# Kernel tuning notes

Hardware: AMD Instinct MI355X
Metric: run time of the kernel (lower is better)

## Reference

```python
import jax, jax.numpy as jnp
import numpy as np

BATCH = 4096
IN_DIM = 512
OUT_DIM = 512
GRID_SIZE = 5
K = 3


def _extended_grid():
    # Original: grid = linspace(-1, 1, grid_size+1), spacing h = 2/grid_size.
    # The de Boor-Cox recursion in the source indexes up to grid[grid_size+2k],
    # so we extend the uniform grid to the right with the same spacing.
    h = 2.0 / GRID_SIZE
    return (-1.0 + h * jnp.arange(GRID_SIZE + 2 * K + 1)).astype(jnp.float32)


def bspline_basis(x, grid, k):
    """Vectorized de Boor-Cox recursion.
    x: [..., ] floats; returns basis [..., grid_size + k].
    Identical math to the recursive b_spline_basis in the source, but computed
    bottom-up over all knot intervals at once (no redundant recomputation).
    """
    xe = x[..., None]  # [..., 1]
    # degree-0: indicator of half-open knot intervals, [..., n_knots-1]
    B = ((grid[:-1] <= xe) & (xe < grid[1:])).astype(x.dtype)
    for d in range(1, k + 1):
        n = grid.shape[0] - d - 1
        gi, gid = grid[:n], grid[d:d + n]          # grid[i], grid[i+d]
        gi1, gid1 = grid[1:n + 1], grid[d + 1:d + n + 1]  # grid[i+1], grid[i+d+1]
        # uniform grid -> denominators are d*h, never zero
        B = (xe - gi) / (gid - gi) * B[..., :n] + (gid1 - xe) / (gid1 - gi1) * B[..., 1:n + 1]
    return B  # [..., grid_size + k]


def setup_inputs() -> dict:
    key = jax.random.key(0)
    k1, k2 = jax.random.split(key)
    x = jax.random.uniform(k1, (BATCH, IN_DIM), jnp.float32) * 2.0 - 1.0  # in [-1, 1)
    spline_coeff = jax.random.normal(k2, (IN_DIM, OUT_DIM, GRID_SIZE + K), jnp.float32)
    spline_scaling = jnp.ones((IN_DIM, OUT_DIM), jnp.float32)
    return {"x": x, "spline_coeff": spline_coeff, "spline_scaling": spline_scaling}


def reference(x, spline_coeff, spline_scaling):
    grid = _extended_grid()
    basis = bspline_basis(x, grid, K)  # [B, in_dim, grid_size+k]
    # out[b, j] = sum_i scaling[i,j] * sum_g basis[b,i,g] * coeff[i,j,g]
    return jnp.einsum('big,ijg,ij->bj', basis, spline_coeff, spline_scaling)
```

## Files before the change

### kernel.cpp

```cpp
#include <hip/hip_runtime.h>
#include <hip/hip_bf16.h>
#include <stdint.h>


#define BATCH   4096
#define IN_DIM  512
#define OUT_DIM 512
#define KDIM    (IN_DIM * 8)
#define SPLITK  4
#define KSPAN   (KDIM / SPLITK)
#define NKS     (KSPAN / 64)

typedef short short8 __attribute__((ext_vector_type(8)));
typedef float f32x4  __attribute__((ext_vector_type(4)));

#define WAIT_VM8   0xF78
#define WAIT_VM0   0xF70
#define WAIT_LGKM0 0xC07F

__device__ __forceinline__ unsigned short f2bf(float f) {
  union { float f; unsigned int u; } v; v.f = f;
  unsigned int r = v.u + 0x7FFFu + ((v.u >> 16) & 1u);
  return (unsigned short)(r >> 16);
}

__device__ __forceinline__ void bspline_win(float xv, float* w, int* mm) {
  float t = (xv + 1.0f) * 2.5f;
  int m = (int)t;
  m = m < 0 ? 0 : (m > 4 ? 4 : m);
  float u  = t - (float)m;
  float u2 = u * u, u3 = u2 * u, om = 1.0f - u;
  w[0] = om * om * om * (1.0f / 6.0f);
  w[1] = (3.0f * u3 - 6.0f * u2 + 4.0f) * (1.0f / 6.0f);
  w[2] = (-3.0f * u3 + 3.0f * u2 + 3.0f * u + 1.0f) * (1.0f / 6.0f);
  w[3] = u3 * (1.0f / 6.0f);
  *mm = m;
}

__device__ __forceinline__ short8 basis_pack8(float xv) {
  float w[4]; int m;
  bspline_win(xv, w, &m);
  short8 h = {};
#pragma unroll
  for (int g = 0; g < 8; ++g) {
    int d = g - m + 3;
    float v = (d == 0) ? w[0] : (d == 1) ? w[1] : (d == 2) ? w[2] : (d == 3) ? w[3] : 0.0f;
    h[g] = (short)f2bf(v);
  }
  return h;
}

__device__ __forceinline__ void async_load16(const void* g, void* l) {
  __builtin_amdgcn_global_load_lds(
      (__attribute__((address_space(1))) void*)(uintptr_t)g,
      (__attribute__((address_space(3))) void*)(unsigned int)(uintptr_t)l,
      16, 0, 0);
}

__global__ void kan_prep(const float* __restrict__ x,
                         const float* __restrict__ coeff,
                         const float* __restrict__ scaling,
                         unsigned short* __restrict__ Ag,
                         unsigned short* __restrict__ Wt,
                         float* __restrict__ out) {
  const int b = blockIdx.x;
  const int NB_A = (BATCH * IN_DIM) / 256;
  const int NB_W = (IN_DIM * OUT_DIM) / 256;
  if (b < NB_A) {
    int idx = b * 256 + threadIdx.x;
    short8 h = basis_pack8(x[idx]);
    *reinterpret_cast<short8*>(Ag + (size_t)idx * 8) = h;
  } else if (b < NB_A + NB_W) {
    int idx = (b - NB_A) * 256 + threadIdx.x;
    int i = idx >> 9, j = idx & 511;
    float s = scaling[idx];
    const float4* cp = reinterpret_cast<const float4*>(coeff) + (size_t)idx * 2;
    float4 c0 = cp[0], c1 = cp[1];
    short8 h;
    h[0] = (short)f2bf(c0.x * s); h[1] = (short)f2bf(c0.y * s);
    h[2] = (short)f2bf(c0.z * s); h[3] = (short)f2bf(c0.w * s);
    h[4] = (short)f2bf(c1.x * s); h[5] = (short)f2bf(c1.y * s);
    h[6] = (short)f2bf(c1.z * s); h[7] = (short)f2bf(c1.w * s);
    *reinterpret_cast<short8*>(Wt + (size_t)j * KDIM + i * 8) = h;
  } else {
    size_t t = (size_t)(b - NB_A - NB_W) * 256 + threadIdx.x;
    reinterpret_cast<float4*>(out)[t] = make_float4(0.f, 0.f, 0.f, 0.f);
  }
}

__global__ __launch_bounds__(256, 2)
void kan_gemm_s(const unsigned short* __restrict__ Ag,
                const unsigned short* __restrict__ Wt,
                float* __restrict__ out) {
  __shared__ unsigned short As[2][128 * 64];
  __shared__ unsigned short Bs[2][128 * 64];

  const int tid  = threadIdx.x;
  const int lane = tid & 63;
  const int wid  = tid >> 6;
  const int wm = wid >> 1, wn = wid & 1;
  const int ln = lane & 15, quad = lane >> 4;

  const int b    = blockIdx.x;
  const int ks   = b & 3;
  const int mt   = (b >> 2) & 31;
  const int nt   = b >> 7;
  const int row0 = mt * 128;
  const int col0 = nt * 128;
  const int k0   = ks * KSPAN;

  f32x4 acc[4][4] = {};
  short8 af[2][4], bfr[2][4];

  const int lr = lane >> 3;
  const int cg = (lane & 7) ^ lr;

  const unsigned short* aRow = Ag + (size_t)(row0 + wid * 32 + lr) * KDIM + k0 + cg * 8;
  const unsigned short* bRow = Wt + (size_t)(col0 + wid * 32 + lr) * KDIM + k0 + cg * 8;

  auto issue = [&](int kt, int st) {
    const int kk0 = kt * 64;
#pragma unroll
    for (int t = 0; t < 4; ++t) {
      const int rbase = wid * 32 + t * 8;
      async_load16(aRow + (size_t)t * 8 * KDIM + kk0, &As[st][rbase * 64]);
      async_load16(bRow + (size_t)t * 8 * KDIM + kk0, &Bs[st][rbase * 64]);
    }
  };

  auto loadFrags = [&](int st) {
#pragma unroll
    for (int kk = 0; kk < 2; ++kk) {
#pragma unroll
      for (int m = 0; m < 4; ++m) {
        const int r    = wm * 64 + m * 16 + ln;
        const int slot = (kk * 4 + quad) ^ (r & 7);
        af[kk][m] = *reinterpret_cast<const short8*>(&As[st][r * 64 + slot * 8]);
      }
#pragma unroll
      for (int n = 0; n < 4; ++n) {
        const int c    = wn * 64 + n * 16 + ln;
        const int slot = (kk * 4 + quad) ^ (c & 7);
        bfr[kk][n] = *reinterpret_cast<const short8*>(&Bs[st][c * 64 + slot * 8]);
      }
    }
  };

  auto mfmaAll = [&]() {
#pragma unroll
    for (int kk = 0; kk < 2; ++kk)
#pragma unroll
      for (int m = 0; m < 4; ++m)
#pragma unroll
        for (int n = 0; n < 4; ++n)
          acc[m][n] = __builtin_amdgcn_mfma_f32_16x16x32_bf16(af[kk][m], bfr[kk][n], acc[m][n], 0, 0, 0);
  };

  issue(0, 0); issue(1, 1);

  for (int kt = 0; kt < NKS - 1; ++kt) {
    __builtin_amdgcn_s_waitcnt(WAIT_VM8);
    __builtin_amdgcn_s_barrier();
    loadFrags(kt & 1);
    __builtin_amdgcn_s_waitcnt(WAIT_LGKM0);
    __builtin_amdgcn_sched_barrier(0);
    __builtin_amdgcn_s_barrier();
    if (kt + 2 < NKS) issue(kt + 2, kt & 1);
    mfmaAll();
  }
  __builtin_amdgcn_s_waitcnt(WAIT_VM0);
  __builtin_amdgcn_s_barrier();
  loadFrags((NKS - 1) & 1);
  mfmaAll();

#pragma unroll
  for (int m = 0; m < 4; ++m)
#pragma unroll
    for (int n = 0; n < 4; ++n) {
      const int col = col0 + wn * 64 + n * 16 + ln;
#pragma unroll
      for (int r = 0; r < 4; ++r) {
        const int row = row0 + wm * 64 + m * 16 + quad * 4 + r;
        atomicAdd(&out[(size_t)row * OUT_DIM + col], acc[m][n][r]);
      }
    }
}

__global__ __launch_bounds__(256, 2)
void kan_gemm_fb(const float* __restrict__ x, const float* __restrict__ coeff,
                 const float* __restrict__ scaling, float* __restrict__ out) {
  __shared__ unsigned short As[64 * 64];
  __shared__ unsigned short Bs[64 * 64];

  const int tid  = threadIdx.x;
  const int lane = tid & 63;
  const int wid  = tid >> 6;
  const int wm = wid >> 1, wn = wid & 1;
  const int ln = lane & 15, quad = lane >> 4;
  const int row0 = blockIdx.y * 64;
  const int col0 = blockIdx.x * 64;

  f32x4 acc[2][2] = {};

  for (int kt = 0; kt < KDIM / 64; ++kt) {
#pragma unroll
    for (int pp = 0; pp < 2; ++pp) {
      const int p  = tid + pp * 256;
      const int rn = p & 63;
      const int il = p >> 6;
      const int sw = ((il ^ (rn & 7)) * 8);
      short8 ha = basis_pack8(x[(size_t)(row0 + rn) * IN_DIM + kt * 8 + il]);
      *reinterpret_cast<short8*>(&As[rn * 64 + sw]) = ha;
      const float* cbase = coeff + (size_t)(kt * 8 + il) * 4096 + (size_t)(col0 + rn) * 8;
      float4 c0 = reinterpret_cast<const float4*>(cbase)[0];
      float4 c1 = reinterpret_cast<const float4*>(cbase)[1];
      float s = scaling[(size_t)(kt * 8 + il) * OUT_DIM + col0 + rn];
      short8 hb;
      hb[0] = (short)f2bf(c0.x * s); hb[1] = (short)f2bf(c0.y * s);
      hb[2] = (short)f2bf(c0.z * s); hb[3] = (short)f2bf(c0.w * s);
      hb[4] = (short)f2bf(c1.x * s); hb[5] = (short)f2bf(c1.y * s);
      hb[6] = (short)f2bf(c1.z * s); hb[7] = (short)f2bf(c1.w * s);
      *reinterpret_cast<short8*>(&Bs[rn * 64 + sw]) = hb;
    }
    __syncthreads();
#pragma unroll
    for (int kk = 0; kk < 2; ++kk) {
      short8 a2[2], b2[2];
#pragma unroll
      for (int mt = 0; mt < 2; ++mt) {
        const int r  = wm * 32 + mt * 16 + ln;
        const int pc = (kk * 4 + quad) ^ (r & 7);
        a2[mt] = *reinterpret_cast<const short8*>(&As[r * 64 + pc * 8]);
      }
#pragma unroll
      for (int nt = 0; nt < 2; ++nt) {
        const int c  = wn * 32 + nt * 16 + ln;
        const int pc = (kk * 4 + quad) ^ (c & 7);
        b2[nt] = *reinterpret_cast<const short8*>(&Bs[c * 64 + pc * 8]);
      }
#pragma unroll
      for (int mt = 0; mt < 2; ++mt)
#pragma unroll
        for (int nt = 0; nt < 2; ++nt)
          acc[mt][nt] = __builtin_amdgcn_mfma_f32_16x16x32_bf16(a2[mt], b2[nt], acc[mt][nt], 0, 0, 0);
    }
    __syncthreads();
  }
#pragma unroll
  for (int mt = 0; mt < 2; ++mt)
#pragma unroll
    for (int nt = 0; nt < 2; ++nt) {
      const int col = col0 + wn * 32 + nt * 16 + ln;
#pragma unroll
      for (int r = 0; r < 4; ++r) {
        const int row = row0 + wm * 32 + mt * 16 + quad * 4 + r;
        out[(size_t)row * OUT_DIM + col] = acc[mt][nt][r];
      }
    }
}

extern "C" void kernel_launch(void* const* d_in, const int* in_sizes, int n_in,
                              void* d_out, int out_size, void* d_ws, size_t ws_size,
                              hipStream_t stream) {
  const float* x       = (const float*)d_in[0];
  const float* coeff   = (const float*)d_in[1];
  const float* scaling = (const float*)d_in[2];
  float* out = (float*)d_out;

  const size_t offW = (size_t)BATCH * KDIM * 2;
  const size_t need = offW + (size_t)OUT_DIM * KDIM * 2;

  if (ws_size >= need) {
    unsigned short* Ag = (unsigned short*)d_ws;
    unsigned short* Wt = (unsigned short*)((char*)d_ws + offW);
    const int NB = (BATCH * IN_DIM) / 256 + (IN_DIM * OUT_DIM) / 256
                 + (BATCH * OUT_DIM / 4) / 256;
    kan_prep<<<NB, 256, 0, stream>>>(x, coeff, scaling, Ag, Wt, out);
    kan_gemm_s<<<(BATCH / 128) * (OUT_DIM / 128) * SPLITK, 256, 0, stream>>>(Ag, Wt, out);
  } else {
    kan_gemm_fb<<<dim3(OUT_DIM / 64, BATCH / 64), 256, 0, stream>>>(x, coeff, scaling, out);
  }
}
```

Measured before the change: 114.2 us.

## Replace split-K atomic accumulation with partial buffers and last-arriver reduction

Each split-K block now writes its fp32 partial tile to a workspace slice instead of doing atomicAdd into the output, then bumps a per-tile arrival counter. The fourth block to arrive sums the four partials with float4 loads and writes the output directly. This drops the output zero-fill and removes about 2M float atomics. In exchange it adds 32 MB of partial writes and reads, fences, and a larger workspace requirement; if the workspace is too small, execution falls back to the slow kernel.

After: 211.3 us. 85.1% more time.

```diff
diff --git a/kernel.cpp b/kernel.cpp
--- a/kernel.cpp
+++ b/kernel.cpp
@@ -62,7 +62,7 @@
                          const float* __restrict__ scaling,
                          unsigned short* __restrict__ Ag,
                          unsigned short* __restrict__ Wt,
-                         float* __restrict__ out) {
+                         unsigned int* __restrict__ cnt) {
   const int b = blockIdx.x;
   const int NB_A = (BATCH * IN_DIM) / 256;
   const int NB_W = (IN_DIM * OUT_DIM) / 256;
@@ -83,17 +83,19 @@
     h[6] = (short)f2bf(c1.z * s); h[7] = (short)f2bf(c1.w * s);
     *reinterpret_cast<short8*>(Wt + (size_t)j * KDIM + i * 8) = h;
   } else {
-    size_t t = (size_t)(b - NB_A - NB_W) * 256 + threadIdx.x;
-    reinterpret_cast<float4*>(out)[t] = make_float4(0.f, 0.f, 0.f, 0.f);
+    if (threadIdx.x < 128) cnt[threadIdx.x] = 0u;
   }
 }
 
 __global__ __launch_bounds__(256, 2)
 void kan_gemm_s(const unsigned short* __restrict__ Ag,
                 const unsigned short* __restrict__ Wt,
+                float* __restrict__ Pt,
+                unsigned int* __restrict__ cnt,
                 float* __restrict__ out) {
   __shared__ unsigned short As[2][128 * 64];
   __shared__ unsigned short Bs[2][128 * 64];
+  __shared__ unsigned int sArrive;
 
   const int tid  = threadIdx.x;
   const int lane = tid & 63;
@@ -173,6 +175,7 @@
   loadFrags((NKS - 1) & 1);
   mfmaAll();
 
+  float* P = Pt + (size_t)ks * BATCH * OUT_DIM;
 #pragma unroll
   for (int m = 0; m < 4; ++m)
 #pragma unroll
@@ -181,9 +184,33 @@
 #pragma unroll
       for (int r = 0; r < 4; ++r) {
         const int row = row0 + wm * 64 + m * 16 + quad * 4 + r;
-        atomicAdd(&out[(size_t)row * OUT_DIM + col], acc[m][n][r]);
-      }
-    }
+        P[(size_t)row * OUT_DIM + col] = acc[m][n][r];
+      }
+    }
+
+  __threadfence();
+  __syncthreads();
+  if (tid == 0) sArrive = atomicAdd(&cnt[mt * 4 + nt], 1u);
+  __syncthreads();
+  if (sArrive != 3u) return;
+  __threadfence();
+
+  const size_t Q = (size_t)BATCH * OUT_DIM / 4;
+  const float4* p4 = reinterpret_cast<const float4*>(Pt);
+#pragma unroll
+  for (int q = 0; q < 16; ++q) {
+    const int idx = q * 256 + tid;
+    const int r   = idx >> 5;
+    const int c4  = idx & 31;
+    const size_t e = (size_t)(row0 + r) * (OUT_DIM / 4) + (col0 >> 2) + c4;
+    float4 a = p4[e], bb = p4[e + Q], c = p4[e + 2 * Q], d = p4[e + 3 * Q];
+    float4 s;
+    s.x = (a.x + bb.x) + (c.x + d.x);
+    s.y = (a.y + bb.y) + (c.y + d.y);
+    s.z = (a.z + bb.z) + (c.z + d.z);
+    s.w = (a.w + bb.w) + (c.w + d.w);
+    reinterpret_cast<float4*>(out)[e] = s;
+  }
 }
 
 __global__ __launch_bounds__(256, 2)
@@ -268,15 +295,19 @@
   float* out = (float*)d_out;
 
   const size_t offW = (size_t)BATCH * KDIM * 2;
-  const size_t need = offW + (size_t)OUT_DIM * KDIM * 2;
+  const size_t offP = offW + (size_t)OUT_DIM * KDIM * 2;
+  const size_t offC = offP + (size_t)SPLITK * BATCH * OUT_DIM * 4;
+  const size_t need = offC + 128 * sizeof(unsigned int);
 
   if (ws_size >= need) {
     unsigned short* Ag = (unsigned short*)d_ws;
     unsigned short* Wt = (unsigned short*)((char*)d_ws + offW);
-    const int NB = (BATCH * IN_DIM) / 256 + (IN_DIM * OUT_DIM) / 256
-                 + (BATCH * OUT_DIM / 4) / 256;
-    kan_prep<<<NB, 256, 0, stream>>>(x, coeff, scaling, Ag, Wt, out);
-    kan_gemm_s<<<(BATCH / 128) * (OUT_DIM / 128) * SPLITK, 256, 0, stream>>>(Ag, Wt, out);
+    float*          Pt = (float*)((char*)d_ws + offP);
+    unsigned int*  cnt = (unsigned int*)((char*)d_ws + offC);
+    const int NB = (BATCH * IN_DIM) / 256 + (IN_DIM * OUT_DIM) / 256 + 1;
+    kan_prep<<<NB, 256, 0, stream>>>(x, coeff, scaling, Ag, Wt, cnt);
+    kan_gemm_s<<<(BATCH / 128) * (OUT_DIM / 128) * SPLITK, 256, 0, stream>>>(
+        Ag, Wt, Pt, cnt, out);
   } else {
     kan_gemm_fb<<<dim3(OUT_DIM / 64, BATCH / 64), 256, 0, stream>>>(x, coeff, scaling, out);
   }
```
